# Kernel optimization log

Measured on AMD Instinct MI355X. Metric: run time of the kernel, lower is better.

Reference implementation:

```python
import jax, jax.numpy as jnp
import numpy as np

NA, NB_N, ND = 100000, 100000, 50000   # nodes per ntype a, b, d
H, OUT = 128, 16                        # hidden dim, num classes
NUM_BASES, NREL, E = 2, 4, 600000       # basis decomposition, relations, edges/rel
RELS = [('a', 'd'), ('b', 'd'), ('d', 'a'), ('d', 'b')]  # sorted rel canonical types
NT = {'a': NA, 'b': NB_N, 'd': ND}


def setup_inputs() -> dict:
    key = jax.random.key(0)
    ks = jax.random.split(key, 32)
    inp = {
        'feat_a': jax.random.normal(ks[0], (NA, H), jnp.float32),
        'feat_b': jax.random.normal(ks[1], (NB_N, H), jnp.float32),
        'feat_d': jax.random.normal(ks[2], (ND, H), jnp.float32),
    }
    # 3 layers: h->h, h->h, h->out; basis-decomposed relation weights + layer bias
    for l, (din, dout) in enumerate([(H, H), (H, H), (H, OUT)]):
        inp[f'basis{l}'] = jax.random.normal(ks[3 + 3 * l], (NUM_BASES, din, dout), jnp.float32) / np.sqrt(din)
        inp[f'coef{l}'] = jax.random.normal(ks[4 + 3 * l], (NREL, NUM_BASES), jnp.float32)
        inp[f'bias{l}'] = jnp.zeros((dout,), jnp.float32)
    # edge lists per relation (src indexes src-ntype, dst indexes dst-ntype)
    for r, (st, dt) in enumerate(RELS):
        inp[f'e{r}_src'] = jax.random.randint(ks[16 + 2 * r], (E,), 0, NT[st], jnp.int32)
        inp[f'e{r}_dst'] = jax.random.randint(ks[17 + 2 * r], (E,), 0, NT[dt], jnp.int32)
    return inp


def _rel_layer(h, basis, coef, bias, edges, act):
    # W_r = sum_b coef[r,b] * basis[b]  -> [NREL, din, dout]
    W = jnp.einsum('rb,bio->rio', coef, basis)
    dout = W.shape[-1]
    out = {nt: jnp.zeros((n, dout), W.dtype) for nt, n in NT.items()}
    for r, (st, dt) in enumerate(RELS):
        src, dst = edges[r]
        # aggregate-then-transform (linear commutes with the sum): saves FLOPs+memory
        agg = jax.ops.segment_sum(h[st][src], dst, num_segments=NT[dt])  # [Ndt, din]
        deg = jax.ops.segment_sum(jnp.ones((src.shape[0],), W.dtype), dst, num_segments=NT[dt])
        agg = agg / jnp.maximum(deg, 1.0)[:, None]  # norm='right' (in-degree, clamp 1)
        out[dt] = out[dt] + agg @ W[r]
    if act:
        return {k: jax.nn.relu(v + bias) for k, v in out.items()}
    return {k: v + bias for k, v in out.items()}


def reference(feat_a, feat_b, feat_d,
              basis0, coef0, bias0, basis1, coef1, bias1, basis2, coef2, bias2,
              e0_src, e0_dst, e1_src, e1_dst, e2_src, e2_dst, e3_src, e3_dst):
    edges = [(e0_src, e0_dst), (e1_src, e1_dst), (e2_src, e2_dst), (e3_src, e3_dst)]
    h = {'a': feat_a, 'b': feat_b, 'd': feat_d}
    h = _rel_layer(h, basis0, coef0, bias0, edges, True)
    h = _rel_layer(h, basis1, coef1, bias1, edges, True)
    h = _rel_layer(h, basis2, coef2, bias2, edges, False)
    return h['d']  # eval-mode output of EntityClassify
```

## Files before the change

### kernel.cpp

```cpp
#include <hip/hip_runtime.h>

#define NA 100000
#define NB 100000
#define ND 50000
#define HDIM 128
#define DOUT 16
#define NODE_TOT (2*ND + NA + NB)
#define BSH 9
#define BKN 512
#define NBUCKET ((NODE_TOT + BKN - 1) >> BSH)
#define BCAP 8192
#define EPB 4096
#define TP 136

typedef __attribute__((ext_vector_type(8))) short short8v;
typedef __attribute__((ext_vector_type(4))) float f32x4;

__device__ __forceinline__ unsigned short f2bf(float f) {
    unsigned u = __float_as_uint(f);
    return (unsigned short)((u + 0x7fffu + ((u >> 16) & 1u)) >> 16);
}
__device__ __forceinline__ void addbf2(float& x, float& y, unsigned u) {
    x += __uint_as_float(u << 16);
    y += __uint_as_float(u & 0xffff0000u);
}

struct EdgeT { int node; int src; };
__device__ __forceinline__ EdgeT edge_at(int g,
    const int* __restrict__ s0, const int* __restrict__ d0,
    const int* __restrict__ s1, const int* __restrict__ d1,
    const int* __restrict__ s2, const int* __restrict__ d2,
    const int* __restrict__ s3, const int* __restrict__ d3,
    int E0, int E1, int E2) {
    EdgeT e;
    if (g < E0)             { e.node = d0[g];                    e.src = s0[g]; }
    else if (g < E0+E1)     { e.node = ND + d1[g-E0];            e.src = s1[g-E0]; }
    else if (g < E0+E1+E2)  { e.node = 2*ND + d2[g-E0-E1];       e.src = s2[g-E0-E1]; }
    else                    { e.node = 2*ND+NA + d3[g-E0-E1-E2]; e.src = s3[g-E0-E1-E2]; }
    return e;
}

__global__ __launch_bounds__(256) void k_weights(const float* __restrict__ basis,
                                                 const float* __restrict__ coef,
                                                 float* __restrict__ W0, float* __restrict__ W1,
                                                 int r0, int r1, int n) {
    int i = blockIdx.x * 256 + threadIdx.x;
    if (i >= n) return;
    float b0 = basis[i], b1 = basis[n + i];
    W0[i] = coef[r0*2+0]*b0 + coef[r0*2+1]*b1;
    W1[i] = coef[r1*2+0]*b0 + coef[r1*2+1]*b1;
}

__global__ __launch_bounds__(256) void k_weights_bfT(const float* __restrict__ basis,
                                                     const float* __restrict__ coef,
                                                     unsigned short* __restrict__ WT0,
                                                     unsigned short* __restrict__ WT1,
                                                     int r0, int r1) {
    int i = blockIdx.x * 256 + threadIdx.x;
    if (i >= HDIM*HDIM) return;
    int k = i >> 7, j = i & 127;
    float b0 = basis[i], b1 = basis[HDIM*HDIM + i];
    WT0[(size_t)j*HDIM + k] = f2bf(coef[r0*2+0]*b0 + coef[r0*2+1]*b1);
    WT1[(size_t)j*HDIM + k] = f2bf(coef[r1*2+0]*b0 + coef[r1*2+1]*b1);
}

__global__ __launch_bounds__(256) void k_cvt_bf16_ab(const float* __restrict__ ina,
                                                     const float* __restrict__ inb,
                                                     unsigned int* __restrict__ outa,
                                                     unsigned int* __restrict__ outb) {
    int i = blockIdx.x * 256 + threadIdx.x;
    const float* in; unsigned int* out;
    if (i < NA*16) { in = ina; out = outa; }
    else           { in = inb; out = outb; i -= NA*16; }
    const float4 a = *(const float4*)(in + (size_t)i*8);
    const float4 b = *(const float4*)(in + (size_t)i*8 + 4);
    uint4 p;
    p.x = (unsigned)f2bf(a.x) | ((unsigned)f2bf(a.y) << 16);
    p.y = (unsigned)f2bf(a.z) | ((unsigned)f2bf(a.w) << 16);
    p.z = (unsigned)f2bf(b.x) | ((unsigned)f2bf(b.y) << 16);
    p.w = (unsigned)f2bf(b.z) | ((unsigned)f2bf(b.w) << 16);
    *(uint4*)(out + (size_t)i*4) = p;
}

__global__ __launch_bounds__(256) void k_ginit(int* __restrict__ gcur) {
    int i = blockIdx.x * 256 + threadIdx.x;
    if (i < NBUCKET) gcur[i] = i * BCAP;
}

__global__ __launch_bounds__(256) void k_bscatter(const int* __restrict__ s0, const int* __restrict__ d0,
                                                  const int* __restrict__ s1, const int* __restrict__ d1,
                                                  const int* __restrict__ s2, const int* __restrict__ d2,
                                                  const int* __restrict__ s3, const int* __restrict__ d3,
                                                  int E0, int E1, int E2, int Etot,
                                                  int* __restrict__ gcur,
                                                  unsigned int* __restrict__ pairs) {
    __shared__ int hist[NBUCKET];
    __shared__ int base[NBUCKET];
    for (int i = threadIdx.x; i < NBUCKET; i += 256) hist[i] = 0;
    __syncthreads();
    int g0 = blockIdx.x * EPB + threadIdx.x;
    int nd[EPB/256], sr[EPB/256], rk[EPB/256];
    #pragma unroll
    for (int i = 0; i < EPB/256; ++i) {
        int g = g0 + i*256;
        if (g < Etot) {
            EdgeT e = edge_at(g, s0,d0,s1,d1,s2,d2,s3,d3, E0,E1,E2);
            nd[i] = e.node; sr[i] = e.src;
            rk[i] = atomicAdd(&hist[e.node >> BSH], 1);
        } else nd[i] = -1;
    }
    __syncthreads();
    for (int i = threadIdx.x; i < NBUCKET; i += 256)
        if (hist[i]) base[i] = atomicAdd(&gcur[i], hist[i]);
    __syncthreads();
    #pragma unroll
    for (int i = 0; i < EPB/256; ++i) {
        if (nd[i] >= 0) {
            unsigned p = ((unsigned)(nd[i] & (BKN-1)) << 17) | (unsigned)sr[i];
            pairs[base[nd[i] >> BSH] + rk[i]] = p;
        }
    }
}

__global__ __launch_bounds__(256) void k_bdeg(const unsigned int* __restrict__ pairs,
                                              const int* __restrict__ gcur,
                                              int* __restrict__ deg) {
    __shared__ int ld[BKN];
    int b = blockIdx.x;
    for (int i = threadIdx.x; i < BKN; i += 256) ld[i] = 0;
    __syncthreads();
    int j0 = b * BCAP, j1 = gcur[b];
    for (int j = j0 + threadIdx.x; j < j1; j += 256)
        atomicAdd(&ld[pairs[j] >> 17], 1);
    __syncthreads();
    int nbase = b << BSH;
    for (int i = threadIdx.x; i < BKN && nbase + i < NODE_TOT; i += 256)
        deg[nbase + i] = ld[i];
}

__global__ __launch_bounds__(256) void k_bfill(const unsigned int* __restrict__ pairs,
                                               const int* __restrict__ gcur,
                                               const int* __restrict__ offs,
                                               int* __restrict__ csr) {
    __shared__ int cur[BKN];
    int b = blockIdx.x;
    int nbase = b << BSH;
    for (int i = threadIdx.x; i < BKN && nbase + i < NODE_TOT; i += 256)
        cur[i] = offs[nbase + i];
    __syncthreads();
    int j0 = b * BCAP, j1 = gcur[b];
    for (int j = j0 + threadIdx.x; j < j1; j += 256) {
        unsigned e = pairs[j];
        int p = atomicAdd(&cur[e >> 17], 1);
        csr[p] = (int)(e & 0x1FFFFu);
    }
}

__global__ __launch_bounds__(1024) void k_scan1(const int* __restrict__ deg,
                                                int* __restrict__ offs,
                                                int* __restrict__ bsum, int N) {
    __shared__ int sh[1024];
    int i = blockIdx.x * 1024 + threadIdx.x;
    int v = (i < N) ? deg[i] : 0;
    sh[threadIdx.x] = v;
    __syncthreads();
    for (int off = 1; off < 1024; off <<= 1) {
        int t = (threadIdx.x >= off) ? sh[threadIdx.x - off] : 0;
        __syncthreads();
        sh[threadIdx.x] += t;
        __syncthreads();
    }
    if (i < N) offs[i + 1] = sh[threadIdx.x];
    if (threadIdx.x == 1023) bsum[blockIdx.x] = sh[1023];
    if (i == 0) offs[0] = 0;
}

__global__ __launch_bounds__(1024) void k_scan2(int* __restrict__ bsum, int nb) {
    __shared__ int sh[1024];
    int t = threadIdx.x;
    sh[t] = (t < nb) ? bsum[t] : 0;
    __syncthreads();
    for (int off = 1; off < 1024; off <<= 1) {
        int v = (t >= off) ? sh[t - off] : 0;
        __syncthreads();
        sh[t] += v;
        __syncthreads();
    }
    if (t < nb) bsum[t] = sh[t];
}

__global__ __launch_bounds__(1024) void k_scan3(int* __restrict__ offs,
                                                const int* __restrict__ bsum, int N) {
    int i = blockIdx.x * 1024 + threadIdx.x;
    if (blockIdx.x > 0 && i < N) offs[i + 1] += bsum[blockIdx.x - 1];
}

__global__ __launch_bounds__(256) void k_gfused_l0(const unsigned int* __restrict__ fa,
                                                   const unsigned int* __restrict__ fb,
                                                   const int* __restrict__ offs,
                                                   const int* __restrict__ csr,
                                                   const unsigned short* __restrict__ WT0,
                                                   const unsigned short* __restrict__ WT1,
                                                   const float* __restrict__ bias,
                                                   unsigned short* __restrict__ outbf, int nrows) {
    __shared__ unsigned short tA[64 * TP];
    __shared__ unsigned short tB[64 * TP];
    const int t = threadIdx.x;
    const int row0 = blockIdx.x * 64;
    {
        const int q = t & 15;
        const int gslot = t >> 4;
        for (int batch = 0; batch < 8; ++batch) {
            int gr = batch * 16 + gslot;
            int lrow = gr & 63;
            bool isB = gr >= 64;
            const unsigned int* tbl = isB ? fb : fa;
            unsigned short* tile = isB ? tB : tA;
            float a0=0,a1=0,a2=0,a3=0,a4=0,a5=0,a6=0,a7=0;
            int deg = 0;
            if (row0 + lrow < nrows) {
                int node = (isB ? ND : 0) + row0 + lrow;
                int s0 = offs[node];
                deg = offs[node + 1] - s0;
                for (int j = 0; j < deg; j += 16) {
                    int cnt = deg - j; if (cnt > 16) cnt = 16;
                    int myidx = (j + q < deg) ? csr[s0 + j + q] : 0;
                    #pragma unroll
                    for (int k = 0; k < 16; ++k) {
                        if (k < cnt) {
                            int idx = __shfl(myidx, k, 16);
                            uint4 v = *(const uint4*)(tbl + (size_t)idx*64 + q*4);
                            addbf2(a0,a1,v.x); addbf2(a2,a3,v.y); addbf2(a4,a5,v.z); addbf2(a6,a7,v.w);
                        }
                    }
                }
            }
            float sc = 1.0f / fmaxf((float)deg, 1.0f);
            uint4 o;
            o.x = (unsigned)f2bf(a0*sc) | ((unsigned)f2bf(a1*sc) << 16);
            o.y = (unsigned)f2bf(a2*sc) | ((unsigned)f2bf(a3*sc) << 16);
            o.z = (unsigned)f2bf(a4*sc) | ((unsigned)f2bf(a5*sc) << 16);
            o.w = (unsigned)f2bf(a6*sc) | ((unsigned)f2bf(a7*sc) << 16);
            *(uint4*)(tile + lrow*TP + q*8) = o;
        }
    }
    __syncthreads();
    const int l = t & 63;
    const int w = t >> 6;
    const int colw = w * 32;
    const int kl = (l >> 4) * 8;
    const int rl = l & 15;
    f32x4 acc[4][2];
    #pragma unroll
    for (int r = 0; r < 4; ++r) { acc[r][0] = (f32x4)0.f; acc[r][1] = (f32x4)0.f; }
    #pragma unroll
    for (int h = 0; h < 2; ++h) {
        const unsigned short* tile = h ? tB : tA;
        const unsigned short* WT = h ? WT1 : WT0;
        #pragma unroll
        for (int s = 0; s < 4; ++s) {
            const int k0 = s * 32;
            short8v b0 = *(const short8v*)(WT + (size_t)(colw + rl)*HDIM + k0 + kl);
            short8v b1 = *(const short8v*)(WT + (size_t)(colw + 16 + rl)*HDIM + k0 + kl);
            short8v a[4];
            #pragma unroll
            for (int r = 0; r < 4; ++r)
                a[r] = *(const short8v*)(tile + (r*16 + rl)*TP + k0 + kl);
            #pragma unroll
            for (int r = 0; r < 4; ++r) {
                acc[r][0] = __builtin_amdgcn_mfma_f32_16x16x32_bf16(a[r], b0, acc[r][0], 0, 0, 0);
                acc[r][1] = __builtin_amdgcn_mfma_f32_16x16x32_bf16(a[r], b1, acc[r][1], 0, 0, 0);
            }
        }
    }
    const float bc0 = bias[colw + rl];
    const float bc1 = bias[colw + 16 + rl];
    #pragma unroll
    for (int r = 0; r < 4; ++r)
        #pragma unroll
        for (int j = 0; j < 4; ++j) {
            int row = row0 + r*16 + (l >> 4)*4 + j;
            if (row < nrows) {
                outbf[(size_t)row*HDIM + colw + rl]      = f2bf(fmaxf(acc[r][0][j] + bc0, 0.f));
                outbf[(size_t)row*HDIM + colw + 16 + rl] = f2bf(fmaxf(acc[r][1][j] + bc1, 0.f));
            }
        }
}

__global__ __launch_bounds__(256) void k_mfma_dual(const unsigned short* __restrict__ A,
                                                   const unsigned short* __restrict__ WTa,
                                                   const unsigned short* __restrict__ WTb,
                                                   unsigned short* __restrict__ outa,
                                                   unsigned short* __restrict__ outb, int nrows) {
    const unsigned short* WT = blockIdx.y ? WTb : WTa;
    unsigned short* outp = blockIdx.y ? outb : outa;
    const int l = threadIdx.x & 63;
    const int w = threadIdx.x >> 6;
    const int row0 = blockIdx.x * 64;
    const int colw = w * 32;
    const int kl = (l >> 4) * 8;
    const int rl = l & 15;
    f32x4 acc[4][2];
    #pragma unroll
    for (int r = 0; r < 4; ++r) { acc[r][0] = (f32x4)0.f; acc[r][1] = (f32x4)0.f; }
    const short8v az = {0,0,0,0,0,0,0,0};
    #pragma unroll
    for (int s = 0; s < 4; ++s) {
        const int k0 = s * 32;
        short8v b0 = *(const short8v*)(WT + (size_t)(colw + rl)*HDIM + k0 + kl);
        short8v b1 = *(const short8v*)(WT + (size_t)(colw + 16 + rl)*HDIM + k0 + kl);
        short8v a[4];
        #pragma unroll
        for (int r = 0; r < 4; ++r) {
            int row = row0 + r*16 + rl;
            a[r] = (row < nrows) ? *(const short8v*)(A + (size_t)row*HDIM + k0 + kl) : az;
        }
        #pragma unroll
        for (int r = 0; r < 4; ++r) {
            acc[r][0] = __builtin_amdgcn_mfma_f32_16x16x32_bf16(a[r], b0, acc[r][0], 0, 0, 0);
            acc[r][1] = __builtin_amdgcn_mfma_f32_16x16x32_bf16(a[r], b1, acc[r][1], 0, 0, 0);
        }
    }
    #pragma unroll
    for (int r = 0; r < 4; ++r)
        #pragma unroll
        for (int j = 0; j < 4; ++j) {
            int row = row0 + r*16 + (l >> 4)*4 + j;
            if (row < nrows) {
                outp[(size_t)row*HDIM + colw + rl]      = f2bf(acc[r][0][j]);
                outp[(size_t)row*HDIM + colw + 16 + rl] = f2bf(acc[r][1][j]);
            }
        }
}

__global__ __launch_bounds__(256) void k_gather_trans16_ab(const unsigned int* __restrict__ t2,
                                                           const unsigned int* __restrict__ t3,
                                                           const int* __restrict__ offs,
                                                           const int* __restrict__ csr,
                                                           const float* __restrict__ bias,
                                                           const float* __restrict__ W20,
                                                           const float* __restrict__ W21,
                                                           float* __restrict__ t1a,
                                                           float* __restrict__ t1b) {
    __shared__ float WlT[16 * 132];
    __shared__ float vbuf[16 * 132];
    const int t = threadIdx.x;
    const bool blkA = (blockIdx.x < NA/16);
    const float* W = blkA ? W20 : W21;
    {
        const int jj = t & 15, c0 = (t >> 4) * 8;
        #pragma unroll
        for (int i = 0; i < 8; ++i)
            WlT[jj*132 + c0 + i] = W[(size_t)(c0 + i)*DOUT + jj];
    }
    __syncthreads();
    const int w = t >> 6, l = t & 63;
    const int sub = l >> 4, q = l & 15;
    const int lrow = w * 4 + sub;
    const int node = 2*ND + blockIdx.x * 16 + lrow;
    const unsigned int* tbl = blkA ? t2 : t3;
    const int s0 = offs[node];
    const int deg = offs[node + 1] - s0;
    float a0=0,a1=0,a2=0,a3=0,a4=0,a5=0,a6=0,a7=0;
    for (int j = 0; j < deg; j += 16) {
        int cnt = deg - j; if (cnt > 16) cnt = 16;
        int myidx = (j + q < deg) ? csr[s0 + j + q] : 0;
        #pragma unroll
        for (int k = 0; k < 16; ++k) {
            if (k < cnt) {
                int idx = __shfl(myidx, k, 16);
                uint4 v = *(const uint4*)(tbl + (size_t)idx*64 + q*4);
                addbf2(a0,a1,v.x); addbf2(a2,a3,v.y); addbf2(a4,a5,v.z); addbf2(a6,a7,v.w);
            }
        }
    }
    const float sc = 1.0f / fmaxf((float)deg, 1.0f);
    const float4 bi0 = *(const float4*)(bias + q*8);
    const float4 bi1 = *(const float4*)(bias + q*8 + 4);
    float4 v0, v1;
    v0.x = fmaxf(a0*sc + bi0.x, 0.f); v0.y = fmaxf(a1*sc + bi0.y, 0.f);
    v0.z = fmaxf(a2*sc + bi0.z, 0.f); v0.w = fmaxf(a3*sc + bi0.w, 0.f);
    v1.x = fmaxf(a4*sc + bi1.x, 0.f); v1.y = fmaxf(a5*sc + bi1.y, 0.f);
    v1.z = fmaxf(a6*sc + bi1.z, 0.f); v1.w = fmaxf(a7*sc + bi1.w, 0.f);
    *(float4*)(vbuf + lrow*132 + q*8)     = v0;
    *(float4*)(vbuf + lrow*132 + q*8 + 4) = v1;
    __syncthreads();
    const int rr = t >> 4, jj = t & 15;
    const float* vr = vbuf + rr*132;
    const float* wr = WlT + jj*132;
    float4 acc4 = make_float4(0.f, 0.f, 0.f, 0.f);
    #pragma unroll 8
    for (int c4 = 0; c4 < 32; ++c4) {
        const float4 v = *(const float4*)(vr + c4*4);
        const float4 ww = *(const float4*)(wr + c4*4);
        acc4.x += v.x*ww.x; acc4.y += v.y*ww.y; acc4.z += v.z*ww.z; acc4.w += v.w*ww.w;
    }
    float acc = (acc4.x + acc4.y) + (acc4.z + acc4.w);
    const int grow = blockIdx.x * 16 + rr;
    if (blkA) t1a[(size_t)grow*DOUT + jj] = acc;
    else      t1b[(size_t)(grow - NA)*DOUT + jj] = acc;
}

__global__ __launch_bounds__(256) void k_gather16_combine(const float* __restrict__ t0,
                                                          const float* __restrict__ t1,
                                                          const int* __restrict__ offs0,
                                                          const int* __restrict__ offs1,
                                                          const int* __restrict__ csr,
                                                          const float* __restrict__ bias,
                                                          float* __restrict__ out, int nrows) {
    int t = threadIdx.x;
    int row = blockIdx.x * 64 + (t >> 2);
    if (row >= nrows) return;
    int q = t & 3;
    int c = q * 4;
    float4 acc = make_float4(0.f, 0.f, 0.f, 0.f);
    {
        int s0 = offs0[row], deg = offs0[row + 1] - s0;
        for (int j = 0; j < deg; j += 4) {
            int cnt = deg - j; if (cnt > 4) cnt = 4;
            int myidx = (j + q < deg) ? csr[s0 + j + q] : 0;
            #pragma unroll
            for (int k = 0; k < 4; ++k) {
                if (k < cnt) {
                    int s = __shfl(myidx, k, 4);
                    float4 v = *reinterpret_cast<const float4*>(t0 + (size_t)s*DOUT + c);
                    acc.x += v.x; acc.y += v.y; acc.z += v.z; acc.w += v.w;
                }
            }
        }
        float sc = 1.0f / fmaxf((float)deg, 1.0f);
        acc.x *= sc; acc.y *= sc; acc.z *= sc; acc.w *= sc;
    }
    float4 acc2 = make_float4(0.f, 0.f, 0.f, 0.f);
    {
        int u0 = offs1[row], deg = offs1[row + 1] - u0;
        for (int j = 0; j < deg; j += 4) {
            int cnt = deg - j; if (cnt > 4) cnt = 4;
            int myidx = (j + q < deg) ? csr[u0 + j + q] : 0;
            #pragma unroll
            for (int k = 0; k < 4; ++k) {
                if (k < cnt) {
                    int s = __shfl(myidx, k, 4);
                    float4 v = *reinterpret_cast<const float4*>(t1 + (size_t)s*DOUT + c);
                    acc2.x += v.x; acc2.y += v.y; acc2.z += v.z; acc2.w += v.w;
                }
            }
        }
        float sc2 = 1.0f / fmaxf((float)deg, 1.0f);
        acc2.x *= sc2; acc2.y *= sc2; acc2.z *= sc2; acc2.w *= sc2;
    }
    float4 bi = *reinterpret_cast<const float4*>(bias + c);
    acc.x += acc2.x + bi.x; acc.y += acc2.y + bi.y;
    acc.z += acc2.z + bi.z; acc.w += acc2.w + bi.w;
    *reinterpret_cast<float4*>(out + (size_t)row*DOUT + c) = acc;
}

extern "C" void kernel_launch(void* const* d_in, const int* in_sizes, int n_in,
                              void* d_out, int out_size, void* d_ws, size_t ws_size,
                              hipStream_t stream) {
    const float* feat_a = (const float*)d_in[0];
    const float* feat_b = (const float*)d_in[1];
    const float* basis0 = (const float*)d_in[3];
    const float* coef0  = (const float*)d_in[4];
    const float* bias0  = (const float*)d_in[5];
    const float* basis1 = (const float*)d_in[6];
    const float* coef1  = (const float*)d_in[7];
    const float* bias1  = (const float*)d_in[8];
    const float* basis2 = (const float*)d_in[9];
    const float* coef2  = (const float*)d_in[10];
    const float* bias2  = (const float*)d_in[11];
    const int* s0 = (const int*)d_in[12]; const int* d0 = (const int*)d_in[13];
    const int* s1 = (const int*)d_in[14]; const int* d1 = (const int*)d_in[15];
    const int* s2 = (const int*)d_in[16]; const int* d2 = (const int*)d_in[17];
    const int* s3 = (const int*)d_in[18]; const int* d3 = (const int*)d_in[19];
    const int E0 = in_sizes[12], E1 = in_sizes[14], E2 = in_sizes[16], E3 = in_sizes[18];
    const int Etot = E0 + E1 + E2 + E3;

    char* base = (char*)d_ws;
    auto alloc = [&](size_t bytes) { char* p = base; base += (bytes + 255) & ~(size_t)255; return p; };
    unsigned short* WT00 = (unsigned short*)alloc(HDIM*HDIM*2);
    unsigned short* WT01 = (unsigned short*)alloc(HDIM*HDIM*2);
    unsigned short* WT12 = (unsigned short*)alloc(HDIM*HDIM*2);
    unsigned short* WT13 = (unsigned short*)alloc(HDIM*HDIM*2);
    float* W20 = (float*)alloc(HDIM*DOUT*4);
    float* W21 = (float*)alloc(HDIM*DOUT*4);
    int* offs_all = (int*)alloc((NODE_TOT + 1) * 4);
    int* csr_all  = (int*)alloc((size_t)Etot * 4);
    int* bsum     = (int*)alloc(2048 * 4);
    int* deg      = (int*)alloc(NODE_TOT * 4);
    int* gcur     = (int*)alloc(NBUCKET * 4);
    unsigned int* pairs = (unsigned int*)alloc((size_t)NBUCKET * BCAP * 4);
    unsigned int* fa_bf  = (unsigned int*)alloc((size_t)NA*HDIM*2);
    unsigned int* fb_bf  = (unsigned int*)alloc((size_t)NB*HDIM*2);
    unsigned short* h0_bf = (unsigned short*)alloc((size_t)ND*HDIM*2);
    unsigned int* t2_bf  = (unsigned int*)alloc((size_t)ND*HDIM*2);
    unsigned int* t3_bf  = (unsigned int*)alloc((size_t)ND*HDIM*2);
    float* t1a  = (float*)alloc((size_t)NA*DOUT*4);
    float* t1b  = (float*)alloc((size_t)NB*DOUT*4);
    float* out = (float*)d_out;

    const int* offsR[2] = {offs_all, offs_all + ND};
    const int nbE = (Etot + EPB - 1) / EPB;

    k_weights_bfT<<<(HDIM*HDIM+255)/256, 256, 0, stream>>>(basis0, coef0, WT00, WT01, 0, 1);
    k_weights_bfT<<<(HDIM*HDIM+255)/256, 256, 0, stream>>>(basis1, coef1, WT12, WT13, 2, 3);
    k_weights<<<(HDIM*DOUT+255)/256, 256, 0, stream>>>(basis2, coef2, W20, W21, 0, 1, HDIM*DOUT);
    k_cvt_bf16_ab<<<((NA+NB)*16)/256, 256, 0, stream>>>(feat_a, feat_b, fa_bf, fb_bf);

    {
        k_ginit<<<(NBUCKET+255)/256, 256, 0, stream>>>(gcur);
        k_bscatter<<<nbE, 256, 0, stream>>>(s0,d0,s1,d1,s2,d2,s3,d3, E0,E1,E2, Etot, gcur, pairs);
        k_bdeg<<<NBUCKET, 256, 0, stream>>>(pairs, gcur, deg);
        int nb = (NODE_TOT + 1023) / 1024;
        k_scan1<<<nb, 1024, 0, stream>>>(deg, offs_all, bsum, NODE_TOT);
        k_scan2<<<1, 1024, 0, stream>>>(bsum, nb);
        k_scan3<<<nb, 1024, 0, stream>>>(offs_all, bsum, NODE_TOT);
        k_bfill<<<NBUCKET, 256, 0, stream>>>(pairs, gcur, offs_all, csr_all);
    }

    k_gfused_l0<<<(ND+63)/64, 256, 0, stream>>>(fa_bf, fb_bf, offs_all, csr_all,
                                                WT00, WT01, bias0, h0_bf, ND);

    k_mfma_dual<<<dim3((ND+63)/64, 2), 256, 0, stream>>>(h0_bf, WT12, WT13,
                                                         (unsigned short*)t2_bf,
                                                         (unsigned short*)t3_bf, ND);

    k_gather_trans16_ab<<<(NA+NB)/16, 256, 0, stream>>>(t2_bf, t3_bf, offs_all, csr_all,
                                                        bias1, W20, W21, t1a, t1b);

    k_gather16_combine<<<(ND+63)/64, 256, 0, stream>>>(t1a, t1b, offsR[0], offsR[1], csr_all,
                                                       bias2, out, ND);
}
```

Measured before the change: 276.9 us.

## Fuse layer-1 dual transform into layer-0 gather kernel via shared tile

Merges the layer-0 gather+transform kernel and the separate dual MFMA kernel into one. The h0 activation tile stays in shared memory and is multiplied by both layer-1 relation weights directly, so h0 is never written to or re-read from global memory and one launch is dropped. LDS use is halved by reusing a single tile for the a and b halves, at the cost of an extra barrier per half. The work is serialized within each block: both layer-1 products now run after the gather instead of in a separate grid with twice the blocks.

```diff
diff --git a/kernel.cpp b/kernel.cpp
--- a/kernel.cpp
+++ b/kernel.cpp
@@ -195,31 +195,38 @@
     if (blockIdx.x > 0 && i < N) offs[i + 1] += bsum[blockIdx.x - 1];
 }
 
-__global__ __launch_bounds__(256) void k_gfused_l0(const unsigned int* __restrict__ fa,
-                                                   const unsigned int* __restrict__ fb,
-                                                   const int* __restrict__ offs,
-                                                   const int* __restrict__ csr,
-                                                   const unsigned short* __restrict__ WT0,
-                                                   const unsigned short* __restrict__ WT1,
-                                                   const float* __restrict__ bias,
-                                                   unsigned short* __restrict__ outbf, int nrows) {
-    __shared__ unsigned short tA[64 * TP];
-    __shared__ unsigned short tB[64 * TP];
+__global__ __launch_bounds__(256) void k_gfused_l01(const unsigned int* __restrict__ fa,
+                                                    const unsigned int* __restrict__ fb,
+                                                    const int* __restrict__ offs,
+                                                    const int* __restrict__ csr,
+                                                    const unsigned short* __restrict__ WT0,
+                                                    const unsigned short* __restrict__ WT1,
+                                                    const unsigned short* __restrict__ WT12,
+                                                    const unsigned short* __restrict__ WT13,
+                                                    const float* __restrict__ bias,
+                                                    unsigned short* __restrict__ t2out,
+                                                    unsigned short* __restrict__ t3out,
+                                                    int nrows) {
+    __shared__ unsigned short tile[64 * TP];
     const int t = threadIdx.x;
     const int row0 = blockIdx.x * 64;
-    {
-        const int q = t & 15;
-        const int gslot = t >> 4;
-        for (int batch = 0; batch < 8; ++batch) {
-            int gr = batch * 16 + gslot;
-            int lrow = gr & 63;
-            bool isB = gr >= 64;
-            const unsigned int* tbl = isB ? fb : fa;
-            unsigned short* tile = isB ? tB : tA;
+    const int l = t & 63, w = t >> 6;
+    const int colw = w * 32, kl = (l >> 4) * 8, rl = l & 15;
+    const int q = t & 15, gslot = t >> 4;
+
+    f32x4 acc[4][2];
+    #pragma unroll
+    for (int r = 0; r < 4; ++r) { acc[r][0] = (f32x4)0.f; acc[r][1] = (f32x4)0.f; }
+
+    #pragma unroll
+    for (int h = 0; h < 2; ++h) {
+        const unsigned int* tbl = h ? fb : fa;
+        for (int batch = 0; batch < 4; ++batch) {
+            int lrow = batch * 16 + gslot;
             float a0=0,a1=0,a2=0,a3=0,a4=0,a5=0,a6=0,a7=0;
             int deg = 0;
             if (row0 + lrow < nrows) {
-                int node = (isB ? ND : 0) + row0 + lrow;
+                int node = (h ? ND : 0) + row0 + lrow;
                 int s0 = offs[node];
                 deg = offs[node + 1] - s0;
                 for (int j = 0; j < deg; j += 16) {
@@ -243,19 +250,7 @@
             o.w = (unsigned)f2bf(a6*sc) | ((unsigned)f2bf(a7*sc) << 16);
             *(uint4*)(tile + lrow*TP + q*8) = o;
         }
-    }
-    __syncthreads();
-    const int l = t & 63;
-    const int w = t >> 6;
-    const int colw = w * 32;
-    const int kl = (l >> 4) * 8;
-    const int rl = l & 15;
-    f32x4 acc[4][2];
-    #pragma unroll
-    for (int r = 0; r < 4; ++r) { acc[r][0] = (f32x4)0.f; acc[r][1] = (f32x4)0.f; }
-    #pragma unroll
-    for (int h = 0; h < 2; ++h) {
-        const unsigned short* tile = h ? tB : tA;
+        __syncthreads();
         const unsigned short* WT = h ? WT1 : WT0;
         #pragma unroll
         for (int s = 0; s < 4; ++s) {
@@ -272,65 +267,54 @@
                 acc[r][1] = __builtin_amdgcn_mfma_f32_16x16x32_bf16(a[r], b1, acc[r][1], 0, 0, 0);
             }
         }
-    }
-    const float bc0 = bias[colw + rl];
-    const float bc1 = bias[colw + 16 + rl];
+        __syncthreads();
+    }
+    {
+        const float bc0 = bias[colw + rl];
+        const float bc1 = bias[colw + 16 + rl];
+        #pragma unroll
+        for (int r = 0; r < 4; ++r)
+            #pragma unroll
+            for (int j = 0; j < 4; ++j) {
+                int lrow = r*16 + (l >> 4)*4 + j;
+                tile[lrow*TP + colw + rl]      = f2bf(fmaxf(acc[r][0][j] + bc0, 0.f));
+                tile[lrow*TP + colw + 16 + rl] = f2bf(fmaxf(acc[r][1][j] + bc1, 0.f));
+            }
+    }
+    __syncthreads();
     #pragma unroll
-    for (int r = 0; r < 4; ++r)
-        #pragma unroll
-        for (int j = 0; j < 4; ++j) {
-            int row = row0 + r*16 + (l >> 4)*4 + j;
-            if (row < nrows) {
-                outbf[(size_t)row*HDIM + colw + rl]      = f2bf(fmaxf(acc[r][0][j] + bc0, 0.f));
-                outbf[(size_t)row*HDIM + colw + 16 + rl] = f2bf(fmaxf(acc[r][1][j] + bc1, 0.f));
-            }
-        }
-}
-
-__global__ __launch_bounds__(256) void k_mfma_dual(const unsigned short* __restrict__ A,
-                                                   const unsigned short* __restrict__ WTa,
-                                                   const unsigned short* __restrict__ WTb,
-                                                   unsigned short* __restrict__ outa,
-                                                   unsigned short* __restrict__ outb, int nrows) {
-    const unsigned short* WT = blockIdx.y ? WTb : WTa;
-    unsigned short* outp = blockIdx.y ? outb : outa;
-    const int l = threadIdx.x & 63;
-    const int w = threadIdx.x >> 6;
-    const int row0 = blockIdx.x * 64;
-    const int colw = w * 32;
-    const int kl = (l >> 4) * 8;
-    const int rl = l & 15;
-    f32x4 acc[4][2];
-    #pragma unroll
-    for (int r = 0; r < 4; ++r) { acc[r][0] = (f32x4)0.f; acc[r][1] = (f32x4)0.f; }
-    const short8v az = {0,0,0,0,0,0,0,0};
-    #pragma unroll
-    for (int s = 0; s < 4; ++s) {
-        const int k0 = s * 32;
-        short8v b0 = *(const short8v*)(WT + (size_t)(colw + rl)*HDIM + k0 + kl);
-        short8v b1 = *(const short8v*)(WT + (size_t)(colw + 16 + rl)*HDIM + k0 + kl);
-        short8v a[4];
-        #pragma unroll
-        for (int r = 0; r < 4; ++r) {
-            int row = row0 + r*16 + rl;
-            a[r] = (row < nrows) ? *(const short8v*)(A + (size_t)row*HDIM + k0 + kl) : az;
-        }
-        #pragma unroll
-        for (int r = 0; r < 4; ++r) {
-            acc[r][0] = __builtin_amdgcn_mfma_f32_16x16x32_bf16(a[r], b0, acc[r][0], 0, 0, 0);
-            acc[r][1] = __builtin_amdgcn_mfma_f32_16x16x32_bf16(a[r], b1, acc[r][1], 0, 0, 0);
-        }
-    }
-    #pragma unroll
-    for (int r = 0; r < 4; ++r)
-        #pragma unroll
-        for (int j = 0; j < 4; ++j) {
-            int row = row0 + r*16 + (l >> 4)*4 + j;
-            if (row < nrows) {
-                outp[(size_t)row*HDIM + colw + rl]      = f2bf(acc[r][0][j]);
-                outp[(size_t)row*HDIM + colw + 16 + rl] = f2bf(acc[r][1][j]);
-            }
-        }
+    for (int h = 0; h < 2; ++h) {
+        const unsigned short* WT = h ? WT13 : WT12;
+        unsigned short* outp = h ? t3out : t2out;
+        f32x4 acc2[4][2];
+        #pragma unroll
+        for (int r = 0; r < 4; ++r) { acc2[r][0] = (f32x4)0.f; acc2[r][1] = (f32x4)0.f; }
+        #pragma unroll
+        for (int s = 0; s < 4; ++s) {
+            const int k0 = s * 32;
+            short8v b0 = *(const short8v*)(WT + (size_t)(colw + rl)*HDIM + k0 + kl);
+            short8v b1 = *(const short8v*)(WT + (size_t)(colw + 16 + rl)*HDIM + k0 + kl);
+            short8v a[4];
+            #pragma unroll
+            for (int r = 0; r < 4; ++r)
+                a[r] = *(const short8v*)(tile + (r*16 + rl)*TP + k0 + kl);
+            #pragma unroll
+            for (int r = 0; r < 4; ++r) {
+                acc2[r][0] = __builtin_amdgcn_mfma_f32_16x16x32_bf16(a[r], b0, acc2[r][0], 0, 0, 0);
+                acc2[r][1] = __builtin_amdgcn_mfma_f32_16x16x32_bf16(a[r], b1, acc2[r][1], 0, 0, 0);
+            }
+        }
+        #pragma unroll
+        for (int r = 0; r < 4; ++r)
+            #pragma unroll
+            for (int j = 0; j < 4; ++j) {
+                int row = row0 + r*16 + (l >> 4)*4 + j;
+                if (row < nrows) {
+                    outp[(size_t)row*HDIM + colw + rl]      = f2bf(acc2[r][0][j]);
+                    outp[(size_t)row*HDIM + colw + 16 + rl] = f2bf(acc2[r][1][j]);
+                }
+            }
+    }
 }
 
 __global__ __launch_bounds__(256) void k_gather_trans16_ab(const unsigned int* __restrict__ t2,
@@ -492,7 +476,6 @@
     unsigned int* pairs = (unsigned int*)alloc((size_t)NBUCKET * BCAP * 4);
     unsigned int* fa_bf  = (unsigned int*)alloc((size_t)NA*HDIM*2);
     unsigned int* fb_bf  = (unsigned int*)alloc((size_t)NB*HDIM*2);
-    unsigned short* h0_bf = (unsigned short*)alloc((size_t)ND*HDIM*2);
     unsigned int* t2_bf  = (unsigned int*)alloc((size_t)ND*HDIM*2);
     unsigned int* t3_bf  = (unsigned int*)alloc((size_t)ND*HDIM*2);
     float* t1a  = (float*)alloc((size_t)NA*DOUT*4);
@@ -518,12 +501,9 @@
         k_bfill<<<NBUCKET, 256, 0, stream>>>(pairs, gcur, offs_all, csr_all);
     }
 
-    k_gfused_l0<<<(ND+63)/64, 256, 0, stream>>>(fa_bf, fb_bf, offs_all, csr_all,
-                                                WT00, WT01, bias0, h0_bf, ND);
-
-    k_mfma_dual<<<dim3((ND+63)/64, 2), 256, 0, stream>>>(h0_bf, WT12, WT13,
-                                                         (unsigned short*)t2_bf,
-                                                         (unsigned short*)t3_bf, ND);
+    k_gfused_l01<<<(ND+63)/64, 256, 0, stream>>>(fa_bf, fb_bf, offs_all, csr_all,
+                                                 WT00, WT01, WT12, WT13, bias0,
+                                                 (unsigned short*)t2_bf, (unsigned short*)t3_bf, ND);
 
     k_gather_trans16_ab<<<(NA+NB)/16, 256, 0, stream>>>(t2_bf, t3_bf, offs_all, csr_all,
                                                         bias1, W20, W21, t1a, t1b);
```

New measurement: 309.1 us. 1.12x slower.
